# Optimization experiments

Hardware: AMD Instinct MI355X
Metric: run time of the kernel (lower is better)

## Reference

```python
import jax, jax.numpy as jnp
import numpy as np

B, D, N, H = 8, 256, 2048, 4  # batch, d_model, seq_len, heads
HEAD_DIM = D // H


def _proj(x, W, b):
    # Conv1D(kernel_size=1) applied to (b, n, d) == dense over channels.
    # x: (B, D, N); W: (D, D) [in, out]; b: (D,) -> (B, D, N)
    return jnp.einsum('bdn,do->bon', x, W) + b[None, :, None]


def setup_inputs() -> dict:
    key = jax.random.key(0)
    ks = jax.random.split(key, 11)
    s = 0.02
    inp = {
        'query': jax.random.normal(ks[0], (B, D, N), jnp.float32),
        'key':   jax.random.normal(ks[1], (B, D, N), jnp.float32),
        'value': jax.random.normal(ks[2], (B, D, N), jnp.float32),
        'Wq': jax.random.normal(ks[3], (D, D), jnp.float32) * s,
        'bq': jnp.zeros((D,), jnp.float32),
        'Wk': jax.random.normal(ks[4], (D, D), jnp.float32) * s,
        'bk': jnp.zeros((D,), jnp.float32),
        'Wv': jax.random.normal(ks[5], (D, D), jnp.float32) * s,
        'bv': jnp.zeros((D,), jnp.float32),
        'Wm': jax.random.normal(ks[6], (D, D), jnp.float32) * s,
        'bm': jnp.zeros((D,), jnp.float32),
    }
    return inp


def reference(query, key, value, Wq, bq, Wk, bk, Wv, bv, Wm, bm):
    b = query.shape[0]
    # project and split heads: (B, D, N) -> (B, head_dim, H, N)
    # NOTE: TF reshape splits d_model as (head_dim, heads) with head_dim outer.
    q = _proj(query, Wq, bq).reshape(b, HEAD_DIM, H, N)
    k = _proj(key,   Wk, bk).reshape(b, HEAD_DIM, H, N)
    v = _proj(value, Wv, bv).reshape(b, HEAD_DIM, H, N)
    # attention with scale 1/sqrt(head_dim)
    scores = jnp.einsum('bdhn,bdhm->bhnm', q, k) / jnp.sqrt(jnp.asarray(HEAD_DIM, q.dtype))
    prob = jax.nn.softmax(scores, axis=-1)
    x = jnp.einsum('bhnm,bdhm->bdhn', prob, v)  # (B, head_dim, H, N)
    x = x.reshape(b, D, N)
    return _proj(x, Wm, bm)
```

## Files before the change

### kernel.cpp

```cpp
#include <hip/hip_runtime.h>
#include <stdint.h>

#define BB 8
#define DD 256
#define NN 2048
#define HH 4
#define HD 64
#define SCALE_Q 0.18033688011112042f

typedef __attribute__((ext_vector_type(8))) short bf16x8;
typedef __attribute__((ext_vector_type(4))) float f32x4;
typedef __attribute__((ext_vector_type(16))) float f32x16;
typedef __attribute__((ext_vector_type(4))) unsigned short u16x4;


__device__ __forceinline__ void gld16(const void* g, void* l) {
  __builtin_amdgcn_global_load_lds(
      (__attribute__((address_space(1))) void*)(void*)(uintptr_t)(g),
      (__attribute__((address_space(3))) void*)(l), 16, 0, 0);
}

__device__ __forceinline__ unsigned short f2bf(float f) {
  union { float f; unsigned u; } v; v.f = f;
  unsigned lsb = (v.u >> 16) & 1u;
  v.u += 0x7fffu + lsb;
  return (unsigned short)(v.u >> 16);
}


__global__ __launch_bounds__(256) void tcast_x(
    const float* __restrict__ q, const float* __restrict__ k,
    const float* __restrict__ v, unsigned short* __restrict__ oq,
    unsigned short* __restrict__ ok2, unsigned short* __restrict__ ov) {
  __shared__ float t[64][65];
  int z = blockIdx.z, src = z >> 3, b = z & 7;
  const float* ip = (src == 0 ? q : src == 1 ? k : v) + (long)b * DD * NN;
  unsigned short* op = (src == 0 ? oq : src == 1 ? ok2 : ov) + (long)b * NN * DD;
  int c0 = blockIdx.x * 64, r0 = blockIdx.y * 64;
  int id = threadIdx.x;
  int hi4 = id >> 4, lo4 = id & 15;
#pragma unroll
  for (int r = 0; r < 4; r++) {
    int d = r * 16 + hi4;
    float4 vv = *(const float4*)(ip + (long)(r0 + d) * NN + c0 + lo4 * 4);
    t[d][lo4 * 4 + 0] = vv.x;
    t[d][lo4 * 4 + 1] = vv.y;
    t[d][lo4 * 4 + 2] = vv.z;
    t[d][lo4 * 4 + 3] = vv.w;
  }
  __syncthreads();
#pragma unroll
  for (int rr = 0; rr < 4; rr++) {
    int n = rr * 16 + hi4;
    u16x4 o4;
#pragma unroll
    for (int j = 0; j < 4; j++) o4[j] = f2bf(t[lo4 * 4 + j][n]);
    *(u16x4*)(op + (long)(c0 + n) * DD + r0 + lo4 * 4) = o4;
  }
}


__global__ __launch_bounds__(256) void tcast_w(
    const float* __restrict__ Wq, const float* __restrict__ Wk,
    const float* __restrict__ Wv, const float* __restrict__ Wm,
    unsigned short* __restrict__ oWq, unsigned short* __restrict__ oWk,
    unsigned short* __restrict__ oWv, unsigned short* __restrict__ oWm) {
  __shared__ float t[32][33];
  int z = blockIdx.z;
  const float* ip = z == 0 ? Wq : z == 1 ? Wk : z == 2 ? Wv : Wm;
  unsigned short* op = z == 0 ? oWq : z == 1 ? oWk : z == 2 ? oWv : oWm;
  float s = z == 0 ? SCALE_Q : 1.f;
  int c0 = blockIdx.x * 32, r0 = blockIdx.y * 32;
  int tx = threadIdx.x & 31, ty = threadIdx.x >> 5;
#pragma unroll
  for (int rr = 0; rr < 4; rr++) {
    int r = rr * 8 + ty;
    t[r][tx] = ip[(long)(r0 + r) * DD + c0 + tx];
  }
  __syncthreads();
  if (z < 3) {
#pragma unroll
    for (int rr = 0; rr < 4; rr++) {
      int c = rr * 8 + ty;
      int o = c0 + c;
      int jp = ((o & 3) << 6) | (o >> 2);
      op[(long)jp * DD + r0 + tx] = f2bf(s * t[tx][c]);
    }
  } else {
#pragma unroll
    for (int rr = 0; rr < 4; rr++) {
      int c = rr * 8 + ty;
      int d = r0 + tx;
      int kp = ((d & 3) << 6) | (d >> 2);
      op[(long)(c0 + c) * DD + kp] = f2bf(t[tx][c]);
    }
  }
}


#define GEMM_STAGE(kt, buf)                                                    \
  {                                                                            \
    int _kt = (kt);                                                            \
    _Pragma("unroll") for (int c = 0; c < 4; c++) {                            \
      int row = w * 32 + c * 8 + (lane >> 3);                                  \
      int so = ((lane & 7) * 16) ^ ((row & 7) << 4);                           \
      gld16((const char*)Ag + ((long)(i0 + row) * DD + _kt * 64) * 2 + so,     \
            (char*)&At[buf][0] + (w * 32 + c * 8) * 128);                      \
    }                                                                          \
    _Pragma("unroll") for (int c = 0; c < 2; c++) {                            \
      int row = w * 16 + c * 8 + (lane >> 3);                                  \
      int so = ((lane & 7) * 16) ^ ((row & 7) << 4);                           \
      gld16((const char*)Bg + ((long)(j0 + row) * DD + _kt * 64) * 2 + so,     \
            (char*)&Bt[buf][0] + (w * 16 + c * 8) * 128);                      \
    }                                                                          \
  }

#define GEMM_COMPUTE(buf)                                                      \
  _Pragma("unroll") for (int ks = 0; ks < 2; ks++) {                           \
    bf16x8 af[4], bfv[2];                                                      \
    _Pragma("unroll") for (int mi = 0; mi < 4; mi++) {                         \
      int row = wr * 64 + mi * 16 + (lane & 15);                               \
      int off = (ks * 64 + (lane >> 4) * 16) ^ ((row & 7) << 4);               \
      af[mi] = *(const bf16x8*)((const char*)&At[buf][0] + row * 128 + off);   \
    }                                                                          \
    _Pragma("unroll") for (int nj = 0; nj < 2; nj++) {                         \
      int row = wc * 32 + nj * 16 + (lane & 15);                               \
      int off = (ks * 64 + (lane >> 4) * 16) ^ ((row & 7) << 4);               \
      bfv[nj] = *(const bf16x8*)((const char*)&Bt[buf][0] + row * 128 + off);  \
    }                                                                          \
    _Pragma("unroll") for (int mi = 0; mi < 4; mi++)                           \
        _Pragma("unroll") for (int nj = 0; nj < 2; nj++)                       \
            acc[mi][nj] = __builtin_amdgcn_mfma_f32_16x16x32_bf16(             \
                af[mi], bfv[nj], acc[mi][nj], 0, 0, 0);                        \
  }

#define GEMM_MAIN()                                                            \
  f32x4 acc[4][2];                                                             \
  _Pragma("unroll") for (int a = 0; a < 4; a++)                                \
      _Pragma("unroll") for (int c = 0; c < 2; c++)                            \
          acc[a][c] = (f32x4){0.f, 0.f, 0.f, 0.f};                             \
  GEMM_STAGE(0, 0);                                                            \
  __syncthreads();                                                             \
  int buf = 0;                                                                 \
  for (int kt = 0; kt < 4; kt++) {                                             \
    if (kt < 3) GEMM_STAGE(kt + 1, buf ^ 1);                                   \
    GEMM_COMPUTE(buf);                                                         \
    __syncthreads();                                                           \
    buf ^= 1;                                                                  \
  }


__global__ __launch_bounds__(256) void gemm_qkv(
    const unsigned short* __restrict__ Xq, const unsigned short* __restrict__ Xk,
    const unsigned short* __restrict__ Xv, const unsigned short* __restrict__ Wq,
    const unsigned short* __restrict__ Wk, const unsigned short* __restrict__ Wv,
    const float* __restrict__ bq, const float* __restrict__ bk,
    const float* __restrict__ bv, unsigned short* __restrict__ Qh,
    unsigned short* __restrict__ Kh, unsigned short* __restrict__ Vh) {
  __shared__ unsigned short At[2][128 * 64], Bt[2][64 * 64];
  int z = blockIdx.z, proj = z >> 3, bb = z & 7;
  int flat = blockIdx.y * 16 + blockIdx.x;
  const unsigned short *Ag, *Bg;
  const float* bias;
  float bsc = 1.f;
  int i0, j0;
  if (proj == 0) {
    Ag = Xq + (long)bb * NN * DD; Bg = Wq; bias = bq; bsc = SCALE_Q;
    i0 = (flat & 15) * 128; j0 = (flat >> 4) * 64;
  } else if (proj == 1) {
    Ag = Xk + (long)bb * NN * DD; Bg = Wk; bias = bk;
    i0 = (flat & 15) * 128; j0 = (flat >> 4) * 64;
  } else {
    Ag = Wv; Bg = Xv + (long)bb * NN * DD; bias = bv;
    i0 = (flat >> 5) * 128; j0 = (flat & 31) * 64;
  }
  int tid = threadIdx.x, lane = tid & 63, w = tid >> 6;
  int wr = w >> 1, wc = w & 1;

  GEMM_MAIN();

#pragma unroll
  for (int mi = 0; mi < 4; mi++) {
#pragma unroll
    for (int nj = 0; nj < 2; nj++) {
#pragma unroll
      for (int r = 0; r < 4; r++) {
        int ig = i0 + wr * 64 + mi * 16 + (lane >> 4) * 4 + r;
        int jg = j0 + wc * 32 + nj * 16 + (lane & 15);
        float v = acc[mi][nj][r];
        if (proj < 2) {
          int o = ((jg & 63) << 2) | (jg >> 6);
          v += bias[o] * bsc;
          int hh = jg >> 6, hd = jg & 63;
          unsigned short* dst = proj == 0 ? Qh : Kh;
          dst[(((long)bb * HH + hh) * NN + ig) * HD + hd] = f2bf(v);
        } else {
          int o = ((ig & 63) << 2) | (ig >> 6);
          v += bias[o];
          int hh = ig >> 6, hd = ig & 63;
          Vh[(((long)bb * HH + hh) * HD + hd) * NN + jg] = f2bf(v);
        }
      }
    }
  }
}


__global__ __launch_bounds__(256) void gemm_out(
    const unsigned short* __restrict__ A, const unsigned short* __restrict__ B,
    const float* __restrict__ bias, float* __restrict__ out) {
  __shared__ unsigned short At[2][128 * 64], Bt[2][64 * 64];
  int bb = blockIdx.z;
  int flat = blockIdx.y * 16 + blockIdx.x;
  const unsigned short* Ag = A;
  const unsigned short* Bg = B + (long)bb * NN * DD;
  int i0 = (flat >> 5) * 128, j0 = (flat & 31) * 64;
  int tid = threadIdx.x, lane = tid & 63, w = tid >> 6;
  int wr = w >> 1, wc = w & 1;

  GEMM_MAIN();

#pragma unroll
  for (int mi = 0; mi < 4; mi++) {
#pragma unroll
    for (int nj = 0; nj < 2; nj++) {
#pragma unroll
      for (int r = 0; r < 4; r++) {
        int ig = i0 + wr * 64 + mi * 16 + (lane >> 4) * 4 + r;
        int jg = j0 + wc * 32 + nj * 16 + (lane & 15);
        out[((long)bb * DD + ig) * NN + jg] = acc[mi][nj][r] + bias[ig];
      }
    }
  }
}


__global__ __launch_bounds__(256) void attn_kernel(
    const unsigned short* __restrict__ Q, const unsigned short* __restrict__ Kg,
    const unsigned short* __restrict__ V, unsigned short* __restrict__ XA) {
  __shared__ unsigned short Kt[2][64 * 64];
  __shared__ unsigned short Vt[2][64 * 64];
  int flat = blockIdx.x;
  int work = (flat & 7) * 64 + (flat >> 3);
  int qb = work & 15, hbid = work >> 4;
  int h = hbid & 3, b = hbid >> 2;
  int tid = threadIdx.x, lane = tid & 63, w = tid >> 6;
  int l31 = lane & 31, hi = lane >> 5;
  int q0 = qb * 128 + w * 32;
  long hb = (long)b * HH + h;
  const unsigned short* Qb = Q + hb * NN * HD;
  const unsigned short* Kb = Kg + hb * NN * HD;
  const unsigned short* Vb = V + hb * HD * NN;

  const f32x16 FZ = {0.f, 0.f, 0.f, 0.f, 0.f, 0.f, 0.f, 0.f,
                     0.f, 0.f, 0.f, 0.f, 0.f, 0.f, 0.f, 0.f};

  bf16x8 qf[4];
#pragma unroll
  for (int ks = 0; ks < 4; ks++)
    qf[ks] = *(const bf16x8*)(Qb + (long)(q0 + l31) * HD + ks * 16 + hi * 8);

  f32x16 oA[2];
#pragma unroll
  for (int hf = 0; hf < 2; hf++)
#pragma unroll
    for (int r = 0; r < 16; r++) oA[hf][r] = 0.f;
  float lsum = 0.f;

  auto stage = [&](int buf, int t) {
    int m0 = t * 64;
#pragma unroll
    for (int c = 0; c < 2; c++) {
      int row = w * 16 + c * 8 + (lane >> 3);
      int so = ((lane & 7) * 16) ^ ((row & 7) << 4);
      gld16((const char*)Kb + (long)(m0 + row) * 128 + so,
            (char*)&Kt[buf][0] + (w * 16 + c * 8) * 128);
      gld16((const char*)Vb + ((long)row * NN + m0) * 2 + so,
            (char*)&Vt[buf][0] + (w * 16 + c * 8) * 128);
    }
  };

  int cur = 0;
  stage(0, 0);
  __syncthreads();

  for (int t = 0; t < NN / 64; t++) {
    if (t + 1 < NN / 64) stage(cur ^ 1, t + 1);

#pragma unroll
    for (int kh = 0; kh < 2; kh++) {
      f32x16 s;
#pragma unroll
      for (int ks = 0; ks < 4; ks++) {
        int row = kh * 32 + l31;
        int off = (ks * 32 + hi * 16) ^ ((row & 7) << 4);
        bf16x8 kf = *(const bf16x8*)((const char*)&Kt[cur][0] + row * 128 + off);
        s = __builtin_amdgcn_mfma_f32_32x32x16_bf16(kf, qf[ks],
                                                    ks == 0 ? FZ : s, 0, 0, 0);
      }
      float p[16];
#pragma unroll
      for (int r = 0; r < 16; r++) {
        p[r] = __builtin_amdgcn_exp2f(s[r]);
        lsum += p[r];
      }
      unsigned pk[8];
#pragma unroll
      for (int i = 0; i < 8; i++)
        asm("v_cvt_pk_bf16_f32 %0, %1, %2"
            : "=v"(pk[i]) : "v"(p[2 * i]), "v"(p[2 * i + 1]));
      asm volatile("v_permlane32_swap_b32 %0, %1" : "+v"(pk[0]), "+v"(pk[2]));
      asm volatile("v_permlane32_swap_b32 %0, %1" : "+v"(pk[1]), "+v"(pk[3]));
      asm volatile("v_permlane32_swap_b32 %0, %1" : "+v"(pk[4]), "+v"(pk[6]));
      asm volatile("v_permlane32_swap_b32 %0, %1" : "+v"(pk[5]), "+v"(pk[7]));
#pragma unroll
      for (int sv = 0; sv < 2; sv++) {
        union { bf16x8 v; unsigned u[4]; } fr;
        fr.u[0] = pk[sv * 4 + 0]; fr.u[1] = pk[sv * 4 + 1];
        fr.u[2] = pk[sv * 4 + 2]; fr.u[3] = pk[sv * 4 + 3];
#pragma unroll
        for (int hf = 0; hf < 2; hf++) {
          int vrow = hf * 32 + l31;
          int voff = ((2 * kh + sv) * 32 + hi * 16) ^ ((vrow & 7) << 4);
          bf16x8 vf = *(const bf16x8*)((const char*)&Vt[cur][0] + vrow * 128 + voff);
          oA[hf] = __builtin_amdgcn_mfma_f32_32x32x16_bf16(fr.v, vf, oA[hf], 0, 0, 0);
        }
      }
    }
    __syncthreads();
    cur ^= 1;
  }

  float lt = lsum + __shfl_xor(lsum, 32);
#pragma unroll
  for (int r = 0; r < 16; r++) {
    int qrow = (r & 3) + 8 * (r >> 2) + 4 * hi;
    float linv = 1.0f / __shfl(lt, qrow);
    long nrow = (long)b * NN + q0 + qrow;
#pragma unroll
    for (int hf = 0; hf < 2; hf++) {
      float val = oA[hf][r] * linv;
      XA[nrow * DD + h * HD + hf * 32 + l31] = f2bf(val);
    }
  }
}


extern "C" void kernel_launch(void* const* d_in, const int* in_sizes, int n_in,
                              void* d_out, int out_size, void* d_ws, size_t ws_size,
                              hipStream_t stream) {
  const float* q_in = (const float*)d_in[0];
  const float* k_in = (const float*)d_in[1];
  const float* v_in = (const float*)d_in[2];
  const float* Wq = (const float*)d_in[3];
  const float* bq = (const float*)d_in[4];
  const float* Wk = (const float*)d_in[5];
  const float* bk = (const float*)d_in[6];
  const float* Wv = (const float*)d_in[7];
  const float* bv = (const float*)d_in[8];
  const float* Wm = (const float*)d_in[9];
  const float* bm = (const float*)d_in[10];
  float* out = (float*)d_out;

  const long SX = (long)BB * NN * DD;
  const long SW = (long)DD * DD;
  unsigned short* Xqt = (unsigned short*)d_ws;
  unsigned short* Xkt = Xqt + SX;
  unsigned short* Xvt = Xkt + SX;
  unsigned short* Qh = Xvt + SX;
  unsigned short* Kh = Qh + SX;
  unsigned short* Vh = Kh + SX;
  unsigned short* Wqt = Vh + SX;
  unsigned short* Wkt = Wqt + SW;
  unsigned short* Wvt = Wkt + SW;
  unsigned short* Wmt = Wvt + SW;
  unsigned short* XAt = Xqt;
  if (ws_size < (size_t)(6 * SX + 4 * SW) * 2) return;

  dim3 blk(256);
  tcast_x<<<dim3(NN / 64, DD / 64, 24), blk, 0, stream>>>(
      q_in, k_in, v_in, Xqt, Xkt, Xvt);
  tcast_w<<<dim3(DD / 32, DD / 32, 4), blk, 0, stream>>>(
      Wq, Wk, Wv, Wm, Wqt, Wkt, Wvt, Wmt);
  gemm_qkv<<<dim3(16, 4, 24), blk, 0, stream>>>(
      Xqt, Xkt, Xvt, Wqt, Wkt, Wvt, bq, bk, bv, Qh, Kh, Vh);
  attn_kernel<<<dim3(512), blk, 0, stream>>>(Qh, Kh, Vh, XAt);
  gemm_out<<<dim3(16, 4, 8), blk, 0, stream>>>(Wmt, XAt, bm, out);
}
```

Before: 192.0 us.

## Split attention key range across two wave groups per block and merge partials

Doubles the attention block to 512 threads. The two groups of four waves each process half of the key/value sequence for the same 128 queries, each with its own double-buffered LDS tiles. Partial outputs and row sums are merged through LDS at the end, and the per-tile row-sum accumulation becomes a tree reduction. The goal is more waves in flight per CU to hide latency, since the grid of 512 blocks is small relative to the CU count. The cost is twice the LDS, an extra merge barrier with an LDS round-trip, and a higher register-pressure bound from the launch-bounds change.

```diff
diff --git a/kernel.cpp b/kernel.cpp
--- a/kernel.cpp
+++ b/kernel.cpp
@@ -235,18 +235,19 @@
 }
 
 
-__global__ __launch_bounds__(256) void attn_kernel(
+__global__ __launch_bounds__(512, 4) void attn_kernel(
     const unsigned short* __restrict__ Q, const unsigned short* __restrict__ Kg,
     const unsigned short* __restrict__ V, unsigned short* __restrict__ XA) {
-  __shared__ unsigned short Kt[2][64 * 64];
-  __shared__ unsigned short Vt[2][64 * 64];
+  __shared__ unsigned short Kt[2][2][64 * 64];
+  __shared__ unsigned short Vt[2][2][64 * 64];
   int flat = blockIdx.x;
   int work = (flat & 7) * 64 + (flat >> 3);
   int qb = work & 15, hbid = work >> 4;
   int h = hbid & 3, b = hbid >> 2;
   int tid = threadIdx.x, lane = tid & 63, w = tid >> 6;
+  int qs = w & 3, half = w >> 2;
   int l31 = lane & 31, hi = lane >> 5;
-  int q0 = qb * 128 + w * 32;
+  int q0 = qb * 128 + qs * 32;
   long hb = (long)b * HH + h;
   const unsigned short* Qb = Q + hb * NN * HD;
   const unsigned short* Kb = Kg + hb * NN * HD;
@@ -271,21 +272,22 @@
     int m0 = t * 64;
 #pragma unroll
     for (int c = 0; c < 2; c++) {
-      int row = w * 16 + c * 8 + (lane >> 3);
+      int row = qs * 16 + c * 8 + (lane >> 3);
       int so = ((lane & 7) * 16) ^ ((row & 7) << 4);
       gld16((const char*)Kb + (long)(m0 + row) * 128 + so,
-            (char*)&Kt[buf][0] + (w * 16 + c * 8) * 128);
+            (char*)&Kt[half][buf][0] + (qs * 16 + c * 8) * 128);
       gld16((const char*)Vb + ((long)row * NN + m0) * 2 + so,
-            (char*)&Vt[buf][0] + (w * 16 + c * 8) * 128);
+            (char*)&Vt[half][buf][0] + (qs * 16 + c * 8) * 128);
     }
   };
 
+  const int HT = NN / 64 / 2;
   int cur = 0;
-  stage(0, 0);
+  stage(0, half * HT);
   __syncthreads();
 
-  for (int t = 0; t < NN / 64; t++) {
-    if (t + 1 < NN / 64) stage(cur ^ 1, t + 1);
+  for (int tt = 0; tt < HT; tt++) {
+    if (tt + 1 < HT) stage(cur ^ 1, half * HT + tt + 1);
 
 #pragma unroll
     for (int kh = 0; kh < 2; kh++) {
@@ -294,16 +296,16 @@
       for (int ks = 0; ks < 4; ks++) {
         int row = kh * 32 + l31;
         int off = (ks * 32 + hi * 16) ^ ((row & 7) << 4);
-        bf16x8 kf = *(const bf16x8*)((const char*)&Kt[cur][0] + row * 128 + off);
+        bf16x8 kf = *(const bf16x8*)((const char*)&Kt[half][cur][0] + row * 128 + off);
         s = __builtin_amdgcn_mfma_f32_32x32x16_bf16(kf, qf[ks],
                                                     ks == 0 ? FZ : s, 0, 0, 0);
       }
       float p[16];
 #pragma unroll
-      for (int r = 0; r < 16; r++) {
-        p[r] = __builtin_amdgcn_exp2f(s[r]);
-        lsum += p[r];
-      }
+      for (int r = 0; r < 16; r++) p[r] = __builtin_amdgcn_exp2f(s[r]);
+      float t0 = ((p[0] + p[1]) + (p[2] + p[3])) + ((p[4] + p[5]) + (p[6] + p[7]));
+      float t1 = ((p[8] + p[9]) + (p[10] + p[11])) + ((p[12] + p[13]) + (p[14] + p[15]));
+      lsum += t0 + t1;
       unsigned pk[8];
 #pragma unroll
       for (int i = 0; i < 8; i++)
@@ -322,7 +324,7 @@
         for (int hf = 0; hf < 2; hf++) {
           int vrow = hf * 32 + l31;
           int voff = ((2 * kh + sv) * 32 + hi * 16) ^ ((vrow & 7) << 4);
-          bf16x8 vf = *(const bf16x8*)((const char*)&Vt[cur][0] + vrow * 128 + voff);
+          bf16x8 vf = *(const bf16x8*)((const char*)&Vt[half][cur][0] + vrow * 128 + voff);
           oA[hf] = __builtin_amdgcn_mfma_f32_32x32x16_bf16(fr.v, vf, oA[hf], 0, 0, 0);
         }
       }
@@ -331,16 +333,35 @@
     cur ^= 1;
   }
 
-  float lt = lsum + __shfl_xor(lsum, 32);
-#pragma unroll
-  for (int r = 0; r < 16; r++) {
-    int qrow = (r & 3) + 8 * (r >> 2) + 4 * hi;
-    float linv = 1.0f / __shfl(lt, qrow);
-    long nrow = (long)b * NN + q0 + qrow;
-#pragma unroll
-    for (int hf = 0; hf < 2; hf++) {
-      float val = oA[hf][r] * linv;
-      XA[nrow * DD + h * HD + hf * 32 + l31] = f2bf(val);
+  float* mrgO = (float*)&Kt[0][0][0];
+  float* mrgL = (float*)&Vt[0][0][0];
+  if (half == 1) {
+#pragma unroll
+    for (int hf = 0; hf < 2; hf++)
+#pragma unroll
+      for (int r = 0; r < 16; r++)
+        mrgO[qs * 2048 + hf * 1024 + r * 64 + lane] = oA[hf][r];
+    mrgL[qs * 64 + lane] = lsum;
+  }
+  __syncthreads();
+  if (half == 0) {
+#pragma unroll
+    for (int hf = 0; hf < 2; hf++)
+#pragma unroll
+      for (int r = 0; r < 16; r++)
+        oA[hf][r] += mrgO[qs * 2048 + hf * 1024 + r * 64 + lane];
+    lsum += mrgL[qs * 64 + lane];
+    float lt = lsum + __shfl_xor(lsum, 32);
+#pragma unroll
+    for (int r = 0; r < 16; r++) {
+      int qrow = (r & 3) + 8 * (r >> 2) + 4 * hi;
+      float linv = 1.0f / __shfl(lt, qrow);
+      long nrow = (long)b * NN + q0 + qrow;
+#pragma unroll
+      for (int hf = 0; hf < 2; hf++) {
+        float val = oA[hf][r] * linv;
+        XA[nrow * DD + h * HD + hf * 32 + l31] = f2bf(val);
+      }
     }
   }
 }
@@ -384,6 +405,6 @@
       Wq, Wk, Wv, Wm, Wqt, Wkt, Wvt, Wmt);
   gemm_qkv<<<dim3(16, 4, 24), blk, 0, stream>>>(
       Xqt, Xkt, Xvt, Wqt, Wkt, Wvt, bq, bk, bv, Qh, Kh, Vh);
-  attn_kernel<<<dim3(512), blk, 0, stream>>>(Qh, Kh, Vh, XAt);
+  attn_kernel<<<dim3(512), dim3(512), 0, stream>>>(Qh, Kh, Vh, XAt);
   gemm_out<<<dim3(16, 4, 8), blk, 0, stream>>>(Wmt, XAt, bm, out);
 }
```

Result: faster. 182.8 us (-4.8%).
